# Kernel optimization log

Measured on AMD Instinct MI355X. Metric: run time of the kernel, lower is better.

The kernel has to match this reference:

```python
import jax, jax.numpy as jnp
import numpy as np

N_HEAD = 16

def _proj1x1(W, b, x):
    # kernel-size-1 Conv1d == channel-wise linear: x (B, C_in, T) -> (B, C_out, T)
    return jnp.einsum('oc,bct->bot', W, x) + b[None, :, None]

def setup_inputs() -> dict:
    key = jax.random.key(0)
    B, C, T = 2, 512, 2048
    ks = jax.random.split(key, 11)
    s = 0.02
    return {
        'q': jax.random.normal(ks[0], (B, C, T), jnp.float32),
        'k': jax.random.normal(ks[1], (B, C, T), jnp.float32),
        'v': jax.random.normal(ks[2], (B, C, T), jnp.float32),
        'mask': jnp.ones((B, 1, T), dtype=bool),
        'Wq': jax.random.normal(ks[3], (C, C), jnp.float32) * s,
        'bq': jax.random.normal(ks[4], (C,), jnp.float32) * s,
        'Wk': jax.random.normal(ks[5], (C, C), jnp.float32) * s,
        'bk': jax.random.normal(ks[6], (C,), jnp.float32) * s,
        'Wv': jax.random.normal(ks[7], (C, C), jnp.float32) * s,
        'bv': jax.random.normal(ks[8], (C,), jnp.float32) * s,
        'Wp': jax.random.normal(ks[9], (C, C), jnp.float32) * s,
        'bp': jax.random.normal(ks[10], (C,), jnp.float32) * s,
    }

def reference(q, k, v, mask, Wq, bq, Wk, bk, Wv, bv, Wp, bp):
    B, C, T = q.shape
    H = N_HEAD
    D = C // H
    scale = 1.0 / np.sqrt(D).astype(np.float32)
    # 1x1 conv projections, then split heads: (B,C,T) -> (B,H,T,D)
    qh = _proj1x1(Wq, bq, q).reshape(B, H, D, T).swapaxes(2, 3)
    kh = _proj1x1(Wk, bk, k).reshape(B, H, D, T).swapaxes(2, 3)
    vh = _proj1x1(Wv, bv, v).reshape(B, H, D, T).swapaxes(2, 3)
    # scores (B,H,Tq,Tk) with key-side mask
    att = jnp.einsum('bhqd,bhkd->bhqk', qh * scale, kh)
    att = jnp.where(mask[:, :, None, :], att, -jnp.inf)
    att = jax.nn.softmax(att, axis=-1)
    # value masking (as in original: v * mask before AV matmul)
    vm = vh * mask[:, :, :, None].astype(vh.dtype)
    out = jnp.einsum('bhqk,bhkd->bhqd', att, vm)
    out = out.swapaxes(2, 3).reshape(B, C, T)
    out = _proj1x1(Wp, bp, out) * mask.astype(out.dtype)
    return (out, mask)
```

## Files before the change

kernel.cpp:

```cpp
#include <hip/hip_runtime.h>

using u16 = unsigned short;
typedef float  f32x4 __attribute__((ext_vector_type(4)));
typedef __bf16 bf8_t __attribute__((ext_vector_type(8)));
typedef u16    u16x4 __attribute__((ext_vector_type(4)));
typedef unsigned int u32x2 __attribute__((ext_vector_type(2)));

#define NB 2
#define NH 16
#define NT 2048
#define ND 32
#define NC 512
#define QK_SCALE 0.17677669529663687f
#define LOG2E    1.4426950408889634f

__device__ __forceinline__ u16 f2bf(float f) {
  unsigned int u = __float_as_uint(f);
  u += 0x7fffu + ((u >> 16) & 1u);
  return (u16)(u >> 16);
}

__device__ __forceinline__ unsigned int cvt_pk_bf16(float a, float b) {
  unsigned int r;
  asm("v_cvt_pk_bf16_f32 %0, %1, %2" : "=v"(r) : "v"(a), "v"(b));
  return r;
}

__device__ __forceinline__ f32x4 mfma16(bf8_t a, bf8_t b, f32x4 c) {
  return __builtin_amdgcn_mfma_f32_16x16x32_bf16(a, b, c, 0, 0, 0);
}

__global__ __launch_bounds__(256) void convert_kernel(
    const float* __restrict__ Wq, const float* __restrict__ Wk,
    const float* __restrict__ Wv, const float* __restrict__ Wp,
    const void* __restrict__ mraw,
    u16* __restrict__ Wc, float* __restrict__ maskf, float* __restrict__ maskb,
    float* __restrict__ outtail) {
  int bid = blockIdx.x;
  if (bid < 1024) {
    int idx = (bid * 256 + (int)threadIdx.x) * 4;
    int m   = idx >> 18;
    int off = idx & 262143;
    const float* W = (m == 0) ? Wq : (m == 1) ? Wk : (m == 2) ? Wv : Wp;
    float s = (m == 0) ? (QK_SCALE * LOG2E) : 1.0f;
    f32x4 wv = *(const f32x4*)(W + off);
    u16x4 pk;
    #pragma unroll
    for (int r = 0; r < 4; ++r) pk[r] = f2bf(wv[r] * s);
    *(u16x4*)(Wc + (size_t)m * (NC * NC) + off) = pk;
  } else {
    unsigned int w0 = *(const unsigned int*)mraw;
    bool intlay = (w0 == 1u);
    #pragma unroll
    for (int kk = 0; kk < 16; ++kk) {
      int j = (int)threadIdx.x + kk * 256;
      float mv;
      if (intlay) mv = ((const int*)mraw)[j] ? 1.0f : 0.0f;
      else        mv = ((const unsigned char*)mraw)[j] ? 1.0f : 0.0f;
      maskf[j]   = mv;
      maskb[j]   = (mv - 1.0f) * 1e30f;
      outtail[j] = mv;
    }
  }
}

__global__ __launch_bounds__(256) void transpose_kernel(
    const float* __restrict__ q, const float* __restrict__ k,
    const float* __restrict__ v, u16* __restrict__ Xt) {
  __shared__ float tile[32][33];
  int z = blockIdx.z;
  int m = z >> 1, b = z & 1;
  const float* src = (m == 0) ? q : (m == 1) ? k : v;
  int t0 = blockIdx.x * 32, c0 = blockIdx.y * 32;
  int tx = threadIdx.x, ty = threadIdx.y;
  #pragma unroll
  for (int j = 0; j < 4; ++j)
    tile[ty + j * 8][tx] = src[(size_t)(b * NC + c0 + ty + j * 8) * NT + t0 + tx];
  __syncthreads();
  u16* dst = Xt + (size_t)m * (NB * NT * NC);
  #pragma unroll
  for (int j = 0; j < 4; ++j)
    dst[((size_t)b * NT + t0 + ty + j * 8) * NC + c0 + tx] = f2bf(tile[tx][ty + j * 8]);
}

__global__ __launch_bounds__(256) void proj_kernel(
    const u16* __restrict__ Wc, const u16* __restrict__ Xt,
    const float* __restrict__ bq, const float* __restrict__ bk, const float* __restrict__ bv,
    u16* __restrict__ Qw, u16* __restrict__ Kw, u16* __restrict__ Vw,
    const float* __restrict__ maskf) {
  int z = blockIdx.z;
  const u16* W = Wc + (size_t)z * (NC * NC);
  const float* bias = (z == 0) ? bq : (z == 1) ? bk : bv;
  int tid = threadIdx.x, wid = tid >> 6, lane = tid & 63;
  int lq = lane & 15, g = lane >> 4;
  int om0 = blockIdx.x * 64;
  int b   = blockIdx.y >> 4;
  int t0  = (blockIdx.y & 15) * 128 + wid * 32;
  const u16* Xb = Xt + (size_t)z * (NB * NT * NC) + (size_t)b * NT * NC;

  const f32x4 zero = {0.f, 0.f, 0.f, 0.f};
  f32x4 acc[4][2];
  #pragma unroll
  for (int mt = 0; mt < 4; ++mt)
    #pragma unroll
    for (int nt = 0; nt < 2; ++nt) acc[mt][nt] = zero;

  for (int ks = 0; ks < 16; ++ks) {
    bf8_t af[4], bfr[2];
    #pragma unroll
    for (int mt = 0; mt < 4; ++mt)
      af[mt] = *(const bf8_t*)(W + (size_t)(om0 + mt * 16 + lq) * NC + ks * 32 + 8 * g);
    #pragma unroll
    for (int nt = 0; nt < 2; ++nt)
      bfr[nt] = *(const bf8_t*)(Xb + (size_t)(t0 + nt * 16 + lq) * NC + ks * 32 + 8 * g);
    #pragma unroll
    for (int mt = 0; mt < 4; ++mt)
      #pragma unroll
      for (int nt = 0; nt < 2; ++nt)
        acc[mt][nt] = mfma16(af[mt], bfr[nt], acc[mt][nt]);
  }

  float sc = (z == 0) ? (QK_SCALE * LOG2E) : 1.0f;
  #pragma unroll
  for (int mt = 0; mt < 4; ++mt) {
    int ob = om0 + mt * 16 + 4 * g;
    float b4[4];
    #pragma unroll
    for (int r = 0; r < 4; ++r) b4[r] = bias[ob + r] * sc;
    #pragma unroll
    for (int nt = 0; nt < 2; ++nt) {
      int t = t0 + nt * 16 + lq;
      if (z < 2) {
        u16x4 pk;
        #pragma unroll
        for (int r = 0; r < 4; ++r) pk[r] = f2bf(acc[mt][nt][r] + b4[r]);
        u16* dst = (z == 0) ? Qw : Kw;
        *(u16x4*)(dst + ((size_t)(b * NH + (ob >> 5)) * NT + t) * ND + (ob & 31)) = pk;
      } else {
        float mv = maskf[b * NT + t];
        #pragma unroll
        for (int r = 0; r < 4; ++r)
          Vw[(size_t)(b * NC + ob + r) * NT + t] = f2bf((acc[mt][nt][r] + b4[r]) * mv);
      }
    }
  }
}

__global__ __launch_bounds__(256) void attn_kernel(
    const u16* __restrict__ Qw, const u16* __restrict__ Kw, const u16* __restrict__ Vw,
    u16* __restrict__ Ow, const float* __restrict__ maskb) {
  __shared__ u16 plds[4][32][128];
  int tid = threadIdx.x, wid = tid >> 6, lane = tid & 63;
  int lq = lane & 15, g = lane >> 4;
  int bh = blockIdx.y, b = bh >> 4, h = bh & 15;
  int q0 = blockIdx.x * 128 + wid * 32;
  const u16* Qb = Qw + (size_t)bh * NT * ND;
  const u16* Kb = Kw + (size_t)bh * NT * ND;
  const u16* Vb = Vw + (size_t)(b * NC + h * ND) * NT;
  const float* mbp = maskb + b * NT;
  char* pbase = (char*)&plds[wid][0][0];

  bf8_t ones;
  #pragma unroll
  for (int j = 0; j < 8; ++j) ones[j] = (__bf16)1.0f;

  bf8_t qf[2];
  #pragma unroll
  for (int c = 0; c < 2; ++c)
    qf[c] = *(const bf8_t*)(Qb + (size_t)(q0 + c * 16 + lq) * ND + 8 * g);

  const f32x4 zero = {0.f, 0.f, 0.f, 0.f};
  f32x4 acc[3][2];
  #pragma unroll
  for (int dt = 0; dt < 3; ++dt)
    #pragma unroll
    for (int c = 0; c < 2; ++c) acc[dt][c] = zero;
  float mrun[2] = {0.f, 0.f};

  for (int kt = 0; kt < 16; ++kt) {
    int tkb = kt * 128;
    f32x4 st[8][2];
    #pragma unroll
    for (int rt = 0; rt < 8; ++rt) {
      f32x4 bias = *(const f32x4*)(mbp + tkb + rt * 16 + 4 * g);
      bf8_t kf = *(const bf8_t*)(Kb + (size_t)(tkb + rt * 16 + lq) * ND + 8 * g);
      st[rt][0] = mfma16(kf, qf[0], bias);
      st[rt][1] = mfma16(kf, qf[1], bias);
    }
    bf8_t vf[2][4];
    #pragma unroll
    for (int dt = 0; dt < 2; ++dt)
      #pragma unroll
      for (int kk = 0; kk < 4; ++kk)
        vf[dt][kk] = *(const bf8_t*)(Vb + (size_t)(dt * 16 + lq) * NT + tkb + kk * 32 + 8 * g);

    #pragma unroll
    for (int c = 0; c < 2; ++c) {
      float tm = -1e30f;
      #pragma unroll
      for (int rt = 0; rt < 8; ++rt) {
        tm = fmaxf(fmaxf(st[rt][c][0], st[rt][c][1]), tm);
        tm = fmaxf(fmaxf(st[rt][c][2], st[rt][c][3]), tm);
      }
      tm = fmaxf(tm, __shfl_xor(tm, 16));
      tm = fmaxf(tm, __shfl_xor(tm, 32));
      if (__any(tm > mrun[c] + 8.0f)) {
        float mnew = fmaxf(mrun[c], tm);
        float al = __builtin_amdgcn_exp2f(mrun[c] - mnew);
        mrun[c] = mnew;
        acc[0][c] *= al; acc[1][c] *= al; acc[2][c] *= al;
      }
      float nm = -mrun[c];
      int row = c * 16 + lq;
      #pragma unroll
      for (int rt = 0; rt < 8; ++rt) {
        float p0 = __builtin_amdgcn_exp2f(st[rt][c][0] + nm);
        float p1 = __builtin_amdgcn_exp2f(st[rt][c][1] + nm);
        float p2 = __builtin_amdgcn_exp2f(st[rt][c][2] + nm);
        float p3 = __builtin_amdgcn_exp2f(st[rt][c][3] + nm);
        u32x2 w;
        w[0] = cvt_pk_bf16(p0, p1);
        w[1] = cvt_pk_bf16(p2, p3);
        *(u32x2*)(pbase + row * 256 + ((rt * 32 + 8 * g) ^ ((row & 7) << 4))) = w;
      }
    }
    #pragma unroll
    for (int kk = 0; kk < 4; ++kk) {
      bf8_t pf[2];
      #pragma unroll
      for (int c = 0; c < 2; ++c) {
        int row = c * 16 + lq;
        pf[c] = *(const bf8_t*)(pbase + row * 256 + ((kk * 64 + 16 * g) ^ ((row & 7) << 4)));
      }
      #pragma unroll
      for (int c = 0; c < 2; ++c) {
        acc[0][c] = mfma16(vf[0][kk], pf[c], acc[0][c]);
        acc[1][c] = mfma16(vf[1][kk], pf[c], acc[1][c]);
        acc[2][c] = mfma16(ones,      pf[c], acc[2][c]);
      }
    }
  }
  #pragma unroll
  for (int c = 0; c < 2; ++c) {
    float inv = 1.0f / acc[2][c][0];
    int t = q0 + c * 16 + lq;
    #pragma unroll
    for (int dt = 0; dt < 2; ++dt) {
      u32x2 o;
      o[0] = cvt_pk_bf16(acc[dt][c][0] * inv, acc[dt][c][1] * inv);
      o[1] = cvt_pk_bf16(acc[dt][c][2] * inv, acc[dt][c][3] * inv);
      *(u32x2*)(Ow + ((size_t)bh * NT + t) * ND + dt * 16 + 4 * g) = o;
    }
  }
}

__global__ __launch_bounds__(256) void outproj_kernel(
    const u16* __restrict__ Wc, const u16* __restrict__ Ow,
    const float* __restrict__ bp, float* __restrict__ out,
    const float* __restrict__ maskf) {
  const u16* W = Wc + (size_t)3 * NC * NC;
  int tid = threadIdx.x, wid = tid >> 6, lane = tid & 63;
  int lq = lane & 15, g = lane >> 4;
  int om0 = blockIdx.x * 64;
  int b   = blockIdx.y >> 4;
  int t0  = (blockIdx.y & 15) * 128 + wid * 32;
  const u16* Ob = Ow + (size_t)b * NH * NT * ND;

  const f32x4 zero = {0.f, 0.f, 0.f, 0.f};
  f32x4 acc[4][2];
  #pragma unroll
  for (int mt = 0; mt < 4; ++mt)
    #pragma unroll
    for (int nt = 0; nt < 2; ++nt) acc[mt][nt] = zero;

  for (int ks = 0; ks < 16; ++ks) {
    bf8_t af[4], bfr[2];
    #pragma unroll
    for (int mt = 0; mt < 4; ++mt)
      af[mt] = *(const bf8_t*)(W + (size_t)(om0 + mt * 16 + lq) * NC + ks * 32 + 8 * g);
    #pragma unroll
    for (int nt = 0; nt < 2; ++nt)
      bfr[nt] = *(const bf8_t*)(Ob + ((size_t)ks * NT + t0 + nt * 16 + lq) * ND + 8 * g);
    #pragma unroll
    for (int mt = 0; mt < 4; ++mt)
      #pragma unroll
      for (int nt = 0; nt < 2; ++nt)
        acc[mt][nt] = mfma16(af[mt], bfr[nt], acc[mt][nt]);
  }
  #pragma unroll
  for (int mt = 0; mt < 4; ++mt) {
    int ob = om0 + mt * 16 + 4 * g;
    float b4[4];
    #pragma unroll
    for (int r = 0; r < 4; ++r) b4[r] = bp[ob + r];
    #pragma unroll
    for (int nt = 0; nt < 2; ++nt) {
      int t = t0 + nt * 16 + lq;
      float mv = maskf[b * NT + t];
      #pragma unroll
      for (int r = 0; r < 4; ++r)
        out[(size_t)(b * NC + ob + r) * NT + t] = (acc[mt][nt][r] + b4[r]) * mv;
    }
  }
}

extern "C" void kernel_launch(void* const* d_in, const int* in_sizes, int n_in,
                              void* d_out, int out_size, void* d_ws, size_t ws_size,
                              hipStream_t stream) {
  const float* q  = (const float*)d_in[0];
  const float* k  = (const float*)d_in[1];
  const float* v  = (const float*)d_in[2];
  const void*  mr = d_in[3];
  const float* Wq = (const float*)d_in[4];
  const float* bq = (const float*)d_in[5];
  const float* Wk = (const float*)d_in[6];
  const float* bk = (const float*)d_in[7];
  const float* Wv = (const float*)d_in[8];
  const float* bv = (const float*)d_in[9];
  const float* Wp = (const float*)d_in[10];
  const float* bp = (const float*)d_in[11];
  float* out = (float*)d_out;

  u16* Wc = (u16*)d_ws;
  u16* Xt = Wc + (size_t)4 * NC * NC;
  u16* Qw = Xt + (size_t)3 * NB * NT * NC;
  u16* Kw = Qw + (size_t)NB * NT * NC;
  u16* Vw = Kw + (size_t)NB * NT * NC;
  u16* Ow = Vw + (size_t)NB * NT * NC;
  float* maskf   = (float*)(Ow + (size_t)NB * NT * NC);
  float* maskb   = maskf + (size_t)NB * NT;
  float* outtail = out + (size_t)NB * NC * NT;

  convert_kernel<<<1025, 256, 0, stream>>>(Wq, Wk, Wv, Wp, mr, Wc, maskf, maskb, outtail);
  transpose_kernel<<<dim3(NT / 32, NC / 32, 6), dim3(32, 8), 0, stream>>>(q, k, v, Xt);
  proj_kernel<<<dim3(8, 32, 3), 256, 0, stream>>>(Wc, Xt, bq, bk, bv, Qw, Kw, Vw, maskf);
  attn_kernel<<<dim3(16, 32), 256, 0, stream>>>(Qw, Kw, Vw, Ow, maskb);
  outproj_kernel<<<dim3(8, 32), 256, 0, stream>>>(Wc, Ow, bp, out, maskf);
}
```

Baseline: 203.9 us.

## Use 32x32 MFMA in attention with register-only P transfer; merge prep kernels

```diff
diff --git a/kernel.cpp b/kernel.cpp
--- a/kernel.cpp
+++ b/kernel.cpp
@@ -1,9 +1,10 @@
 #include <hip/hip_runtime.h>
 
 using u16 = unsigned short;
-typedef float  f32x4 __attribute__((ext_vector_type(4)));
-typedef __bf16 bf8_t __attribute__((ext_vector_type(8)));
-typedef u16    u16x4 __attribute__((ext_vector_type(4)));
+typedef float  f32x4  __attribute__((ext_vector_type(4)));
+typedef float  f32x16 __attribute__((ext_vector_type(16)));
+typedef __bf16 bf8_t  __attribute__((ext_vector_type(8)));
+typedef u16    u16x4  __attribute__((ext_vector_type(4)));
 typedef unsigned int u32x2 __attribute__((ext_vector_type(2)));
 
 #define NB 2
@@ -29,16 +30,24 @@
 __device__ __forceinline__ f32x4 mfma16(bf8_t a, bf8_t b, f32x4 c) {
   return __builtin_amdgcn_mfma_f32_16x16x32_bf16(a, b, c, 0, 0, 0);
 }
-
-__global__ __launch_bounds__(256) void convert_kernel(
+__device__ __forceinline__ f32x16 mfma32(bf8_t a, bf8_t b, f32x16 c) {
+  return __builtin_amdgcn_mfma_f32_32x32x16_bf16(a, b, c, 0, 0, 0);
+}
+
+__global__ __launch_bounds__(256) void prep_kernel(
+    const float* __restrict__ q, const float* __restrict__ k,
+    const float* __restrict__ v, u16* __restrict__ Xt,
     const float* __restrict__ Wq, const float* __restrict__ Wk,
     const float* __restrict__ Wv, const float* __restrict__ Wp,
     const void* __restrict__ mraw,
     u16* __restrict__ Wc, float* __restrict__ maskf, float* __restrict__ maskb,
     float* __restrict__ outtail) {
-  int bid = blockIdx.x;
-  if (bid < 1024) {
-    int idx = (bid * 256 + (int)threadIdx.x) * 4;
+  int z = blockIdx.z;
+  int tx = threadIdx.x, ty = threadIdx.y;
+  if (z == 6) {
+    int bid = blockIdx.y * 64 + blockIdx.x;
+    int tid = ty * 32 + tx;
+    int idx = (bid * 256 + tid) * 4;
     int m   = idx >> 18;
     int off = idx & 262143;
     const float* W = (m == 0) ? Wq : (m == 1) ? Wk : (m == 2) ? Wv : Wp;
@@ -48,31 +57,26 @@
     #pragma unroll
     for (int r = 0; r < 4; ++r) pk[r] = f2bf(wv[r] * s);
     *(u16x4*)(Wc + (size_t)m * (NC * NC) + off) = pk;
-  } else {
-    unsigned int w0 = *(const unsigned int*)mraw;
-    bool intlay = (w0 == 1u);
-    #pragma unroll
-    for (int kk = 0; kk < 16; ++kk) {
-      int j = (int)threadIdx.x + kk * 256;
-      float mv;
-      if (intlay) mv = ((const int*)mraw)[j] ? 1.0f : 0.0f;
-      else        mv = ((const unsigned char*)mraw)[j] ? 1.0f : 0.0f;
-      maskf[j]   = mv;
-      maskb[j]   = (mv - 1.0f) * 1e30f;
-      outtail[j] = mv;
-    }
-  }
-}
-
-__global__ __launch_bounds__(256) void transpose_kernel(
-    const float* __restrict__ q, const float* __restrict__ k,
-    const float* __restrict__ v, u16* __restrict__ Xt) {
+    if (bid == 0) {
+      unsigned int w0 = *(const unsigned int*)mraw;
+      bool intlay = (w0 == 1u);
+      #pragma unroll
+      for (int kk = 0; kk < 16; ++kk) {
+        int j = tid + kk * 256;
+        float mv;
+        if (intlay) mv = ((const int*)mraw)[j] ? 1.0f : 0.0f;
+        else        mv = ((const unsigned char*)mraw)[j] ? 1.0f : 0.0f;
+        maskf[j]   = mv;
+        maskb[j]   = (mv - 1.0f) * 1e30f;
+        outtail[j] = mv;
+      }
+    }
+    return;
+  }
   __shared__ float tile[32][33];
-  int z = blockIdx.z;
   int m = z >> 1, b = z & 1;
   const float* src = (m == 0) ? q : (m == 1) ? k : v;
   int t0 = blockIdx.x * 32, c0 = blockIdx.y * 32;
-  int tx = threadIdx.x, ty = threadIdx.y;
   #pragma unroll
   for (int j = 0; j < 4; ++j)
     tile[ty + j * 8][tx] = src[(size_t)(b * NC + c0 + ty + j * 8) * NT + t0 + tx];
@@ -149,108 +153,107 @@
 __global__ __launch_bounds__(256) void attn_kernel(
     const u16* __restrict__ Qw, const u16* __restrict__ Kw, const u16* __restrict__ Vw,
     u16* __restrict__ Ow, const float* __restrict__ maskb) {
-  __shared__ u16 plds[4][32][128];
   int tid = threadIdx.x, wid = tid >> 6, lane = tid & 63;
-  int lq = lane & 15, g = lane >> 4;
-  int bh = blockIdx.y, b = bh >> 4, h = bh & 15;
+  int lr = lane & 31, hh = lane >> 5;
+  int bh = blockIdx.y, b = bh >> 4, hd = bh & 15;
   int q0 = blockIdx.x * 128 + wid * 32;
   const u16* Qb = Qw + (size_t)bh * NT * ND;
   const u16* Kb = Kw + (size_t)bh * NT * ND;
-  const u16* Vb = Vw + (size_t)(b * NC + h * ND) * NT;
+  const u16* Vb = Vw + (size_t)(b * NC + hd * ND + lr) * NT;
   const float* mbp = maskb + b * NT;
-  char* pbase = (char*)&plds[wid][0][0];
-
-  bf8_t ones;
-  #pragma unroll
-  for (int j = 0; j < 8; ++j) ones[j] = (__bf16)1.0f;
-
-  bf8_t qf[2];
-  #pragma unroll
-  for (int c = 0; c < 2; ++c)
-    qf[c] = *(const bf8_t*)(Qb + (size_t)(q0 + c * 16 + lq) * ND + 8 * g);
-
-  const f32x4 zero = {0.f, 0.f, 0.f, 0.f};
-  f32x4 acc[3][2];
-  #pragma unroll
-  for (int dt = 0; dt < 3; ++dt)
-    #pragma unroll
-    for (int c = 0; c < 2; ++c) acc[dt][c] = zero;
-  float mrun[2] = {0.f, 0.f};
+
+  const u16* Qrow = Qb + (size_t)(q0 + lr) * ND + 8 * hh;
+  bf8_t qf0 = *(const bf8_t*)(Qrow);
+  bf8_t qf1 = *(const bf8_t*)(Qrow + 16);
+
+  f32x16 acc;
+  #pragma unroll
+  for (int r = 0; r < 16; ++r) acc[r] = 0.f;
+  float lsum = 0.f, mrun = 0.f;
 
   for (int kt = 0; kt < 16; ++kt) {
     int tkb = kt * 128;
-    f32x4 st[8][2];
-    #pragma unroll
-    for (int rt = 0; rt < 8; ++rt) {
-      f32x4 bias = *(const f32x4*)(mbp + tkb + rt * 16 + 4 * g);
-      bf8_t kf = *(const bf8_t*)(Kb + (size_t)(tkb + rt * 16 + lq) * ND + 8 * g);
-      st[rt][0] = mfma16(kf, qf[0], bias);
-      st[rt][1] = mfma16(kf, qf[1], bias);
-    }
-    bf8_t vf[2][4];
-    #pragma unroll
-    for (int dt = 0; dt < 2; ++dt)
-      #pragma unroll
-      for (int kk = 0; kk < 4; ++kk)
-        vf[dt][kk] = *(const bf8_t*)(Vb + (size_t)(dt * 16 + lq) * NT + tkb + kk * 32 + 8 * g);
-
-    #pragma unroll
-    for (int c = 0; c < 2; ++c) {
-      float tm = -1e30f;
-      #pragma unroll
-      for (int rt = 0; rt < 8; ++rt) {
-        tm = fmaxf(fmaxf(st[rt][c][0], st[rt][c][1]), tm);
-        tm = fmaxf(fmaxf(st[rt][c][2], st[rt][c][3]), tm);
+    f32x16 st[4];
+    #pragma unroll
+    for (int t = 0; t < 4; ++t) {
+      const float* bb = mbp + tkb + 32 * t + 4 * hh;
+      union { f32x16 v; f32x4 q[4]; } bias;
+      bias.q[0] = *(const f32x4*)(bb);
+      bias.q[1] = *(const f32x4*)(bb + 8);
+      bias.q[2] = *(const f32x4*)(bb + 16);
+      bias.q[3] = *(const f32x4*)(bb + 24);
+      const u16* Kt = Kb + (size_t)(tkb + 32 * t + lr) * ND + 8 * hh;
+      bf8_t k0 = *(const bf8_t*)(Kt);
+      bf8_t k1 = *(const bf8_t*)(Kt + 16);
+      st[t] = mfma32(k0, qf0, bias.v);
+      st[t] = mfma32(k1, qf1, st[t]);
+    }
+    bf8_t vf[4][2];
+    #pragma unroll
+    for (int t = 0; t < 4; ++t)
+      #pragma unroll
+      for (int kh = 0; kh < 2; ++kh)
+        vf[t][kh] = *(const bf8_t*)(Vb + tkb + 32 * t + 16 * kh + 8 * hh);
+
+    float m8[8];
+    #pragma unroll
+    for (int r = 0; r < 8; ++r)
+      m8[r] = fmaxf(fmaxf(st[0][r], st[0][r + 8]), fmaxf(st[1][r], st[1][r + 8]));
+    #pragma unroll
+    for (int r = 0; r < 8; ++r)
+      m8[r] = fmaxf(m8[r], fmaxf(fmaxf(st[2][r], st[2][r + 8]),
+                                 fmaxf(st[3][r], st[3][r + 8])));
+    float tm = fmaxf(fmaxf(fmaxf(m8[0], m8[1]), fmaxf(m8[2], m8[3])),
+                     fmaxf(fmaxf(m8[4], m8[5]), fmaxf(m8[6], m8[7])));
+    tm = fmaxf(tm, __shfl_xor(tm, 32));
+    if (__any(tm > mrun + 2.0f)) {
+      float mnew = fmaxf(mrun, tm);
+      float al = __builtin_amdgcn_exp2f(mrun - mnew);
+      mrun = mnew;
+      #pragma unroll
+      for (int r = 0; r < 16; ++r) acc[r] *= al;
+      lsum *= al;
+    }
+    float nm = -mrun;
+    #pragma unroll
+    for (int t = 0; t < 4; ++t)
+      #pragma unroll
+      for (int r = 0; r < 16; ++r)
+        st[t][r] = __builtin_amdgcn_exp2f(st[t][r] + nm);
+    float s8[8];
+    #pragma unroll
+    for (int r = 0; r < 8; ++r)
+      s8[r] = (st[0][r] + st[0][r + 8]) + (st[1][r] + st[1][r + 8])
+            + (st[2][r] + st[2][r + 8]) + (st[3][r] + st[3][r + 8]);
+    float rs = ((s8[0] + s8[1]) + (s8[2] + s8[3]))
+             + ((s8[4] + s8[5]) + (s8[6] + s8[7]));
+    rs += __shfl_xor(rs, 32);
+    lsum += rs;
+    #pragma unroll
+    for (int t = 0; t < 4; ++t) {
+      #pragma unroll
+      for (int kh = 0; kh < 2; ++kh) {
+        int r0 = kh * 8;
+        unsigned a0 = cvt_pk_bf16(st[t][r0 + 0], st[t][r0 + 1]);
+        unsigned a1 = cvt_pk_bf16(st[t][r0 + 2], st[t][r0 + 3]);
+        unsigned b0 = cvt_pk_bf16(st[t][r0 + 4], st[t][r0 + 5]);
+        unsigned b1 = cvt_pk_bf16(st[t][r0 + 6], st[t][r0 + 7]);
+        asm volatile("v_permlane32_swap_b32 %0, %1" : "+v"(b0), "+v"(a0));
+        asm volatile("v_permlane32_swap_b32 %0, %1" : "+v"(b1), "+v"(a1));
+        union { bf8_t v; unsigned u[4]; } pf;
+        pf.u[0] = a0; pf.u[1] = a1; pf.u[2] = b0; pf.u[3] = b1;
+        acc = mfma32(vf[t][kh], pf.v, acc);
       }
-      tm = fmaxf(tm, __shfl_xor(tm, 16));
-      tm = fmaxf(tm, __shfl_xor(tm, 32));
-      if (__any(tm > mrun[c] + 8.0f)) {
-        float mnew = fmaxf(mrun[c], tm);
-        float al = __builtin_amdgcn_exp2f(mrun[c] - mnew);
-        mrun[c] = mnew;
-        acc[0][c] *= al; acc[1][c] *= al; acc[2][c] *= al;
-      }
-      float nm = -mrun[c];
-      int row = c * 16 + lq;
-      #pragma unroll
-      for (int rt = 0; rt < 8; ++rt) {
-        float p0 = __builtin_amdgcn_exp2f(st[rt][c][0] + nm);
-        float p1 = __builtin_amdgcn_exp2f(st[rt][c][1] + nm);
-        float p2 = __builtin_amdgcn_exp2f(st[rt][c][2] + nm);
-        float p3 = __builtin_amdgcn_exp2f(st[rt][c][3] + nm);
-        u32x2 w;
-        w[0] = cvt_pk_bf16(p0, p1);
-        w[1] = cvt_pk_bf16(p2, p3);
-        *(u32x2*)(pbase + row * 256 + ((rt * 32 + 8 * g) ^ ((row & 7) << 4))) = w;
-      }
-    }
-    #pragma unroll
-    for (int kk = 0; kk < 4; ++kk) {
-      bf8_t pf[2];
-      #pragma unroll
-      for (int c = 0; c < 2; ++c) {
-        int row = c * 16 + lq;
-        pf[c] = *(const bf8_t*)(pbase + row * 256 + ((kk * 64 + 16 * g) ^ ((row & 7) << 4)));
-      }
-      #pragma unroll
-      for (int c = 0; c < 2; ++c) {
-        acc[0][c] = mfma16(vf[0][kk], pf[c], acc[0][c]);
-        acc[1][c] = mfma16(vf[1][kk], pf[c], acc[1][c]);
-        acc[2][c] = mfma16(ones,      pf[c], acc[2][c]);
-      }
-    }
-  }
-  #pragma unroll
-  for (int c = 0; c < 2; ++c) {
-    float inv = 1.0f / acc[2][c][0];
-    int t = q0 + c * 16 + lq;
-    #pragma unroll
-    for (int dt = 0; dt < 2; ++dt) {
-      u32x2 o;
-      o[0] = cvt_pk_bf16(acc[dt][c][0] * inv, acc[dt][c][1] * inv);
-      o[1] = cvt_pk_bf16(acc[dt][c][2] * inv, acc[dt][c][3] * inv);
-      *(u32x2*)(Ow + ((size_t)bh * NT + t) * ND + dt * 16 + 4 * g) = o;
-    }
+    }
+  }
+  float inv = 1.0f / lsum;
+  size_t obase = ((size_t)bh * NT + q0 + lr) * ND + 4 * hh;
+  #pragma unroll
+  for (int c = 0; c < 4; ++c) {
+    u32x2 o;
+    o[0] = cvt_pk_bf16(acc[4 * c + 0] * inv, acc[4 * c + 1] * inv);
+    o[1] = cvt_pk_bf16(acc[4 * c + 2] * inv, acc[4 * c + 3] * inv);
+    *(u32x2*)(Ow + obase + 8 * c) = o;
   }
 }
 
@@ -331,8 +334,8 @@
   float* maskb   = maskf + (size_t)NB * NT;
   float* outtail = out + (size_t)NB * NC * NT;
 
-  convert_kernel<<<1025, 256, 0, stream>>>(Wq, Wk, Wv, Wp, mr, Wc, maskf, maskb, outtail);
-  transpose_kernel<<<dim3(NT / 32, NC / 32, 6), dim3(32, 8), 0, stream>>>(q, k, v, Xt);
+  prep_kernel<<<dim3(64, 16, 7), dim3(32, 8), 0, stream>>>(
+      q, k, v, Xt, Wq, Wk, Wv, Wp, mr, Wc, maskf, maskb, outtail);
   proj_kernel<<<dim3(8, 32, 3), 256, 0, stream>>>(Wc, Xt, bq, bk, bv, Qw, Kw, Vw, maskf);
   attn_kernel<<<dim3(16, 32), 256, 0, stream>>>(Qw, Kw, Vw, Ow, maskb);
   outproj_kernel<<<dim3(8, 32), 256, 0, stream>>>(Wc, Ow, bp, out, maskf);
```

Result: slower. 211.0 us (+3.5%).
